# Performance work log

Hardware: AMD Instinct MI355X
Metric: run time of the kernel (lower is better)

## Reference

```python
import jax, jax.numpy as jnp
import numpy as np

N, INC, MID, K = 65536, 256, 64, 16
EPS = 1e-5  # BatchNorm1d default eps


def _bn(x, g, b, m, v):
    # eval-mode BatchNorm1d applied per-channel along the last dim
    return (x - m) * (g * jax.lax.rsqrt(v + EPS)) + b


def setup_inputs() -> dict:
    key = jax.random.key(0)
    ks = jax.random.split(key, 40)
    rn = lambda i, shape, s=0.05: (jax.random.normal(ks[i], shape, jnp.float32) * s)
    pv = lambda i, n: jax.random.uniform(ks[i], (n,), jnp.float32, 0.5, 1.5)  # positive running var
    return {
        "feats": jax.random.normal(ks[0], (N, INC), jnp.float32),
        "pos": jax.random.uniform(ks[1], (N, 3), jnp.float32) * 10.0,
        "idx": jax.random.randint(ks[2], (N, K), 0, N),
        "w_in": rn(3, (MID, INC)),
        "w_q": rn(4, (MID, MID)), "b_q": rn(5, (MID,)),
        "w_k": rn(6, (MID, MID)), "b_k": rn(7, (MID,)),
        "w_v": rn(8, (MID, MID)), "b_v": rn(9, (MID,)),
        # pos_enc: Linear(3,3) -> BN(3) -> ReLU -> Linear(3,mid) -> BN(mid) -> ReLU
        "pe_w1": rn(10, (3, 3)), "pe_b1": rn(11, (3,)),
        "pe_g1": jnp.ones(3), "pe_be1": rn(12, (3,)), "pe_m1": rn(13, (3,)), "pe_v1": pv(14, 3),
        "pe_w2": rn(15, (MID, 3)), "pe_b2": rn(16, (MID,)),
        "pe_g2": jnp.ones(MID), "pe_be2": rn(17, (MID,)), "pe_m2": rn(18, (MID,)), "pe_v2": pv(19, MID),
        # mlp_gamma: Linear(mid,mid) -> BN(mid) -> ReLU -> Linear(mid,mid) -> BN(mid) -> ReLU
        "ga_w1": rn(20, (MID, MID)), "ga_b1": rn(21, (MID,)),
        "ga_g1": jnp.ones(MID), "ga_be1": rn(22, (MID,)), "ga_m1": rn(23, (MID,)), "ga_v1": pv(24, MID),
        "ga_w2": rn(25, (MID, MID)), "ga_b2": rn(26, (MID,)),
        "ga_g2": jnp.ones(MID), "ga_be2": rn(27, (MID,)), "ga_m2": rn(28, (MID,)), "ga_v2": pv(29, MID),
        "w_out": rn(30, (INC, MID)),
    }


def reference(feats, pos, w_in, w_q, b_q, w_k, b_k, w_v, b_v,
              pe_w1, pe_b1, pe_g1, pe_be1, pe_m1, pe_v1,
              pe_w2, pe_b2, pe_g2, pe_be2, pe_m2, pe_v2,
              ga_w1, ga_b1, ga_g1, ga_be1, ga_m1, ga_v1,
              ga_w2, ga_b2, ga_g2, ga_be2, ga_m2, ga_v2,
              w_out, idx):
    xx = feats @ w_in.T                              # [N, mid]
    q = xx @ w_q.T + b_q
    k = xx @ w_k.T + b_k
    v = xx @ w_v.T + b_v
    xv = v[idx]                                      # [N, K, mid] gather
    xk = k[idx]                                      # [N, K, mid]
    xpos = pos[idx]                                  # [N, K, 3]
    # pos_enc
    p = jax.nn.relu(_bn(xpos @ pe_w1.T + pe_b1, pe_g1, pe_be1, pe_m1, pe_v1))
    p = jax.nn.relu(_bn(p @ pe_w2.T + pe_b2, pe_g2, pe_be2, pe_m2, pe_v2))  # [N, K, mid]
    # vector attention logits
    w = xk - q[:, None, :] + p                       # [N, K, mid]
    # mlp_gamma
    w = jax.nn.relu(_bn(w @ ga_w1.T + ga_b1, ga_g1, ga_be1, ga_m1, ga_v1))
    w = jax.nn.relu(_bn(w @ ga_w2.T + ga_b2, ga_g2, ga_be2, ga_m2, ga_v2))
    w = jax.nn.softmax(w, axis=1)                    # softmax over neighbors
    out = jnp.sum((xv + p) * w, axis=1)              # [N, mid]
    out = out @ w_out.T                              # [N, inc]
    return out + feats
```

## Files before the change

kernel.cpp:

```cpp
#include <hip/hip_runtime.h>

#define NPTS 65536
#define INC  256
#define MID  64
#define KNB  16
#define WSTR 72

#define WIN_S   0
#define WQ_S    16384
#define WK_S    20480
#define WV_S    24576
#define GA1_S   28672
#define GA2_S   32768
#define WOUT_S  36864
#define NFRAG_ENT 6656
#define BQ1F_S  53248

typedef __attribute__((ext_vector_type(8))) short short8;
typedef __attribute__((ext_vector_type(4))) float f32x4;

#define MFMA(a, b, c) __builtin_amdgcn_mfma_f32_16x16x32_bf16((a), (b), (c), 0, 0, 0)
#define WBAR() __builtin_amdgcn_wave_barrier()

__device__ inline float bf2f(unsigned short s) {
    unsigned int u = ((unsigned int)s) << 16;
    return __builtin_bit_cast(float, u);
}
__device__ inline unsigned int pk_bf16(float lo, float hi) {
    unsigned int r;
    asm("v_cvt_pk_bf16_f32 %0, %1, %2" : "=v"(r) : "v"(lo), "v"(hi));
    return r;
}
__device__ inline short f2bf(float f) { return (short)pk_bf16(f, f); }

__device__ inline short8 cvtf8(f32x4 a, f32x4 b) {
    union { unsigned int u[4]; short8 s; } r;
    r.u[0] = pk_bf16(a[0], a[1]); r.u[1] = pk_bf16(a[2], a[3]);
    r.u[2] = pk_bf16(b[0], b[1]); r.u[3] = pk_bf16(b[2], b[3]);
    return r.s;
}
__device__ inline short8 load_cvt8(const float* __restrict__ p) {
    const f32x4* v = (const f32x4*)p;
    return cvtf8(v[0], v[1]);
}
__device__ inline short8 load_cvt8s(const float* __restrict__ p, float scale) {
    const f32x4* v = (const f32x4*)p;
    f32x4 a = v[0], b = v[1];
    #pragma unroll
    for (int i = 0; i < 4; i++) { a[i] *= scale; b[i] *= scale; }
    return cvtf8(a, b);
}

__global__ __launch_bounds__(256) void k_prep(
    const float* __restrict__ w_in, const float* __restrict__ w_q,
    const float* __restrict__ w_k, const float* __restrict__ w_v,
    const float* __restrict__ ga_w1, const float* __restrict__ ga_w2,
    const float* __restrict__ w_out, const float* __restrict__ b_q,
    const float* __restrict__ ga_g1, const float* __restrict__ ga_v1,
    const float* __restrict__ ga_b1, const float* __restrict__ ga_be1,
    const float* __restrict__ ga_m1,
    const float* __restrict__ ga_g2, const float* __restrict__ ga_v2,
    short* __restrict__ wbuf)
{
    int gid = blockIdx.x * 256 + threadIdx.x;
    if (gid >= NFRAG_ENT + 64) return;
    if (gid < 2048) {
        int e = gid, f = e >> 6, ln = e & 63;
        int nt = f & 3, ks = f >> 2;
        int row = nt * 16 + (ln & 15), col = ks * 32 + (ln >> 4) * 8;
        *(short8*)&wbuf[(size_t)gid * 8] = load_cvt8(w_in + (size_t)row * INC + col);
    } else if (gid < 4608) {
        int seg = (gid - 2048) >> 9;
        int e = (gid - 2048) & 511;
        int f = e >> 6, ln = e & 63;
        int nt = f & 3, ks = f >> 2;
        int row = nt * 16 + (ln & 15), col = ks * 32 + (ln >> 4) * 8;
        if (seg == 0) {
            float s1r = ga_g1[row] * rsqrtf(ga_v1[row] + 1e-5f);
            float accv[8];
            #pragma unroll
            for (int o = 0; o < 8; o++) accv[o] = 0.f;
            for (int c = 0; c < 64; c++) {
                float a = ga_w1[(size_t)row * MID + c] * s1r;
                #pragma unroll
                for (int o = 0; o < 8; o++)
                    accv[o] += a * w_q[(size_t)c * MID + col + o];
            }
            f32x4 lo = {accv[0], accv[1], accv[2], accv[3]};
            f32x4 hi = {accv[4], accv[5], accv[6], accv[7]};
            *(short8*)&wbuf[(size_t)gid * 8] = cvtf8(lo, hi);
        } else {
            const float* m = seg == 1 ? w_k : seg == 2 ? w_v
                           : seg == 3 ? ga_w1 : ga_w2;
            float scale = 1.f;
            if (seg == 3)      scale = ga_g1[row] * rsqrtf(ga_v1[row] + 1e-5f);
            else if (seg == 4) scale = ga_g2[row] * rsqrtf(ga_v2[row] + 1e-5f);
            *(short8*)&wbuf[(size_t)gid * 8] = load_cvt8s(m + (size_t)row * MID + col, scale);
        }
    } else if (gid < NFRAG_ENT) {
        int e = gid - 4608, f = e >> 6, ln = e & 63;
        int nt = f >> 1, ks = f & 1;
        int row = nt * 16 + (ln & 15), col = ks * 32 + (ln >> 4) * 8;
        *(short8*)&wbuf[(size_t)gid * 8] = load_cvt8(w_out + (size_t)row * MID + col);
    } else {
        int ch = gid - NFRAG_ENT;
        float s1r = ga_g1[ch] * rsqrtf(ga_v1[ch] + 1e-5f);
        float acc = 0.f;
        for (int c = 0; c < 64; c++) acc += ga_w1[(size_t)ch * MID + c] * b_q[c];
        float beta1 = (ga_b1[ch] - ga_m1[ch]) * s1r + ga_be1[ch];
        ((float*)(wbuf + BQ1F_S))[ch] = s1r * acc - beta1;
    }
}

__global__ __launch_bounds__(256) void k_qkv(
    const float* __restrict__ feats, const short* __restrict__ wfrag,
    const float* __restrict__ pos,
    const float* __restrict__ b_k, const float* __restrict__ b_v,
    const float* __restrict__ pe_w1, const float* __restrict__ pe_b1,
    const float* __restrict__ pe_g1, const float* __restrict__ pe_be1,
    const float* __restrict__ pe_m1, const float* __restrict__ pe_v1,
    const float* __restrict__ pe_w2, const float* __restrict__ pe_b2,
    const float* __restrict__ pe_g2, const float* __restrict__ pe_be2,
    const float* __restrict__ pe_m2, const float* __restrict__ pe_v2,
    short* __restrict__ q1f_out, unsigned* __restrict__ kv_out)
{
    __shared__ __align__(16) short XL[4][16 * WSTR];
    __shared__ float PS[4][16 * 4];
    const int tid = threadIdx.x;
    const int wave = tid >> 6, lane = tid & 63;
    const int l15 = lane & 15, quad = lane >> 4;
    const int rb = (blockIdx.x * 4 + wave) * 16;

    if (lane < 16) {
        float s0 = pe_g1[0] * rsqrtf(pe_v1[0] + 1e-5f);
        float s1 = pe_g1[1] * rsqrtf(pe_v1[1] + 1e-5f);
        float sc = pe_g1[2] * rsqrtf(pe_v1[2] + 1e-5f);
        float px = pos[(size_t)(rb + lane) * 3 + 0];
        float py = pos[(size_t)(rb + lane) * 3 + 1];
        float pz = pos[(size_t)(rb + lane) * 3 + 2];
        PS[wave][lane * 4 + 0] =
            fmaxf((px * pe_w1[0] + py * pe_w1[1] + pz * pe_w1[2] + pe_b1[0] - pe_m1[0]) * s0 + pe_be1[0], 0.f);
        PS[wave][lane * 4 + 1] =
            fmaxf((px * pe_w1[3] + py * pe_w1[4] + pz * pe_w1[5] + pe_b1[1] - pe_m1[1]) * s1 + pe_be1[1], 0.f);
        PS[wave][lane * 4 + 2] =
            fmaxf((px * pe_w1[6] + py * pe_w1[7] + pz * pe_w1[8] + pe_b1[2] - pe_m1[2]) * sc + pe_be1[2], 0.f);
    }

    const float* bq1f = (const float*)(wfrag + BQ1F_S);
    float w2c0[4], w2c1[4], w2c2[4], s2c[4], sh2c[4], bq1c[4], bkc[4], bvc[4];
    #pragma unroll
    for (int nt = 0; nt < 4; nt++) {
        int ch = nt * 16 + l15;
        w2c0[nt] = pe_w2[ch * 3 + 0]; w2c1[nt] = pe_w2[ch * 3 + 1]; w2c2[nt] = pe_w2[ch * 3 + 2];
        float s2 = pe_g2[ch] * rsqrtf(pe_v2[ch] + 1e-5f);
        s2c[nt] = s2;
        sh2c[nt] = (pe_b2[ch] - pe_m2[ch]) * s2 + pe_be2[ch];
        bq1c[nt] = bq1f[ch];
        bkc[nt] = b_k[ch]; bvc[nt] = b_v[ch];
    }

    f32x4 acc[4];
    #pragma unroll
    for (int nt = 0; nt < 4; nt++) acc[nt] = (f32x4){0.f, 0.f, 0.f, 0.f};
    const float* arow = feats + (size_t)(rb + l15) * INC + quad * 8;
    #pragma unroll
    for (int ks = 0; ks < 8; ks++) {
        short8 a = load_cvt8(arow + ks * 32);
        #pragma unroll
        for (int nt = 0; nt < 4; nt++) {
            short8 b = *(const short8*)&wfrag[WIN_S + (size_t)((ks * 4 + nt) * 64 + lane) * 8];
            acc[nt] = MFMA(a, b, acc[nt]);
        }
    }
    #pragma unroll
    for (int nt = 0; nt < 4; nt++) {
        unsigned int p01 = pk_bf16(acc[nt][0], acc[nt][1]);
        unsigned int p23 = pk_bf16(acc[nt][2], acc[nt][3]);
        XL[wave][(quad * 4 + 0) * WSTR + nt * 16 + l15] = (short)p01;
        XL[wave][(quad * 4 + 1) * WSTR + nt * 16 + l15] = (short)(p01 >> 16);
        XL[wave][(quad * 4 + 2) * WSTR + nt * 16 + l15] = (short)p23;
        XL[wave][(quad * 4 + 3) * WSTR + nt * 16 + l15] = (short)(p23 >> 16);
    }
    WBAR();
    short8 a0 = *(const short8*)&XL[wave][l15 * WSTR + quad * 8];
    short8 a1 = *(const short8*)&XL[wave][l15 * WSTR + 32 + quad * 8];
    WBAR();

    float p10[4], p11[4], p12[4];
    #pragma unroll
    for (int r = 0; r < 4; r++) {
        p10[r] = PS[wave][(quad * 4 + r) * 4 + 0];
        p11[r] = PS[wave][(quad * 4 + r) * 4 + 1];
        p12[r] = PS[wave][(quad * 4 + r) * 4 + 2];
    }
    float pe_[4][4];
    #pragma unroll
    for (int nt = 0; nt < 4; nt++)
        #pragma unroll
        for (int r = 0; r < 4; r++)
            pe_[nt][r] = fmaxf((p10[r] * w2c0[nt] + p11[r] * w2c1[nt] + p12[r] * w2c2[nt])
                               * s2c[nt] + sh2c[nt], 0.f);

    #pragma unroll
    for (int nt = 0; nt < 4; nt++) {
        short8 b0 = *(const short8*)&wfrag[WQ_S + (size_t)((nt) * 64 + lane) * 8];
        short8 b1 = *(const short8*)&wfrag[WQ_S + (size_t)((4 + nt) * 64 + lane) * 8];
        f32x4 c = (f32x4){0.f, 0.f, 0.f, 0.f};
        c = MFMA(a0, b0, c); c = MFMA(a1, b1, c);
        unsigned int p01 = pk_bf16(c[0] + bq1c[nt], c[1] + bq1c[nt]);
        unsigned int p23 = pk_bf16(c[2] + bq1c[nt], c[3] + bq1c[nt]);
        q1f_out[(unsigned)(rb + quad * 4 + 0) * 64u + nt * 16 + l15] = (short)p01;
        q1f_out[(unsigned)(rb + quad * 4 + 1) * 64u + nt * 16 + l15] = (short)(p01 >> 16);
        q1f_out[(unsigned)(rb + quad * 4 + 2) * 64u + nt * 16 + l15] = (short)p23;
        q1f_out[(unsigned)(rb + quad * 4 + 3) * 64u + nt * 16 + l15] = (short)(p23 >> 16);
    }

    WBAR();
    #pragma unroll
    for (int nt = 0; nt < 4; nt++) {
        short8 b0 = *(const short8*)&wfrag[WK_S + (size_t)((nt) * 64 + lane) * 8];
        short8 b1 = *(const short8*)&wfrag[WK_S + (size_t)((4 + nt) * 64 + lane) * 8];
        f32x4 c = (f32x4){0.f, 0.f, 0.f, 0.f};
        c = MFMA(a0, b0, c); c = MFMA(a1, b1, c);
        unsigned int p01 = pk_bf16(c[0] + bkc[nt] + pe_[nt][0], c[1] + bkc[nt] + pe_[nt][1]);
        unsigned int p23 = pk_bf16(c[2] + bkc[nt] + pe_[nt][2], c[3] + bkc[nt] + pe_[nt][3]);
        XL[wave][(quad * 4 + 0) * WSTR + nt * 16 + l15] = (short)p01;
        XL[wave][(quad * 4 + 1) * WSTR + nt * 16 + l15] = (short)(p01 >> 16);
        XL[wave][(quad * 4 + 2) * WSTR + nt * 16 + l15] = (short)p23;
        XL[wave][(quad * 4 + 3) * WSTR + nt * 16 + l15] = (short)(p23 >> 16);
    }
    WBAR();
    short8 ak0 = *(const short8*)&XL[wave][l15 * WSTR + quad * 8];
    short8 ak1 = *(const short8*)&XL[wave][l15 * WSTR + 32 + quad * 8];
    WBAR();
    float k1f[4][4];
    #pragma unroll
    for (int nt = 0; nt < 4; nt++) {
        short8 b0 = *(const short8*)&wfrag[GA1_S + (size_t)((nt) * 64 + lane) * 8];
        short8 b1 = *(const short8*)&wfrag[GA1_S + (size_t)((4 + nt) * 64 + lane) * 8];
        f32x4 c = (f32x4){0.f, 0.f, 0.f, 0.f};
        c = MFMA(ak0, b0, c); c = MFMA(ak1, b1, c);
        #pragma unroll
        for (int r = 0; r < 4; r++) k1f[nt][r] = c[r];
    }

    #pragma unroll
    for (int nt = 0; nt < 4; nt++) {
        short8 b0 = *(const short8*)&wfrag[WV_S + (size_t)((nt) * 64 + lane) * 8];
        short8 b1 = *(const short8*)&wfrag[WV_S + (size_t)((4 + nt) * 64 + lane) * 8];
        f32x4 c = (f32x4){0.f, 0.f, 0.f, 0.f};
        c = MFMA(a0, b0, c); c = MFMA(a1, b1, c);
        #pragma unroll
        for (int r = 0; r < 4; r++) {
            float vv = c[r] + bvc[nt] + pe_[nt][r];
            kv_out[(unsigned)(rb + quad * 4 + r) * 64u + nt * 16 + l15] =
                pk_bf16(k1f[nt][r], vv);
        }
    }
}

#define GATHER(KVN, IT2)                                                      \
    _Pragma("unroll")                                                         \
    for (int j = 0; j < KNB; j++) {                                           \
        int mj = __builtin_amdgcn_readlane(m_all, (IT2) * 16 + j);            \
        KVN[j] = kvbuf[(unsigned)mj * 64u + (unsigned)lane];                  \
    }

#define ATTN_POINT(IT, KV, QV, WB)                                            \
    {                                                                         \
        short* wb_ = (WB);                                                    \
        _Pragma("unroll")                                                     \
        for (int j = 0; j < KNB; j += 2) {                                    \
            float h0 = fmaxf(__builtin_bit_cast(float, KV[j] << 16) - (QV), 0.f);     \
            float h1 = fmaxf(__builtin_bit_cast(float, KV[j + 1] << 16) - (QV), 0.f); \
            unsigned pkw = pk_bf16(h0, h1);                                   \
            wb_[(j) * WSTR + lane] = (short)pkw;                              \
            wb_[(j + 1) * WSTR + lane] = (short)(pkw >> 16);                  \
        }                                                                     \
        short8 c0 = *(const short8*)&wb_[l15 * WSTR + quad * 8];              \
        short8 c1 = *(const short8*)&wb_[l15 * WSTR + 32 + quad * 8];         \
        float smv[4][4];                                                      \
        _Pragma("unroll")                                                     \
        for (int nt = 0; nt < 4; nt++) {                                      \
            short8 b0 = *(const short8*)&BW[(size_t)((nt) * 64 + lane) * 8];  \
            short8 b1 = *(const short8*)&BW[(size_t)((4 + nt) * 64 + lane) * 8]; \
            f32x4 c = (f32x4){0.f, 0.f, 0.f, 0.f};                            \
            c = MFMA(c0, b0, c); c = MFMA(c1, b1, c);                         \
            float b2v = B2[nt * 16 + l15];                                    \
            _Pragma("unroll")                                                 \
            for (int r = 0; r < 4; r++)                                       \
                smv[nt][r] = fmaxf(c[r] + b2v, 0.f);                          \
        }                                                                     \
        float sarr[4];                                                        \
        _Pragma("unroll")                                                     \
        for (int nt = 0; nt < 4; nt++) {                                      \
            float e0 = __expf(smv[nt][0]), e1 = __expf(smv[nt][1]);           \
            float e2 = __expf(smv[nt][2]), e3 = __expf(smv[nt][3]);           \
            float s = e0 + e1 + e2 + e3;                                      \
            s += __shfl_xor(s, 16);                                           \
            s += __shfl_xor(s, 32);                                           \
            sarr[nt] = s;                                                     \
            unsigned p01 = pk_bf16(e0, e1);                                   \
            unsigned p23 = pk_bf16(e2, e3);                                   \
            wb_[(quad * 4 + 0) * WSTR + nt * 16 + l15] = (short)p01;          \
            wb_[(quad * 4 + 1) * WSTR + nt * 16 + l15] = (short)(p01 >> 16);  \
            wb_[(quad * 4 + 2) * WSTR + nt * 16 + l15] = (short)p23;          \
            wb_[(quad * 4 + 3) * WSTR + nt * 16 + l15] = (short)(p23 >> 16);  \
        }                                                                     \
        float oacc = 0.f;                                                     \
        _Pragma("unroll")                                                     \
        for (int j = 0; j < KNB; j++)                                         \
            oacc += __builtin_bit_cast(float, KV[j] & 0xffff0000u)            \
                    * bf2f((unsigned short)wb_[j * WSTR + lane]);             \
        float s01 = (quad == 0) ? sarr[0] : sarr[1];                          \
        float s23 = (quad == 2) ? sarr[2] : sarr[3];                          \
        float ssel = (quad < 2) ? s01 : s23;                                  \
        OM[((IT) * 4 + wave) * WSTR + lane] = f2bf(oacc * (1.0f / ssel));     \
    }

__global__ __launch_bounds__(256) void k_attn(
    const int* __restrict__ idx,
    const unsigned short* __restrict__ q1f,
    const unsigned* __restrict__ kvbuf, const short* __restrict__ wfrag,
    const float* __restrict__ ga_b2, const float* __restrict__ ga_g2,
    const float* __restrict__ ga_be2, const float* __restrict__ ga_m2,
    const float* __restrict__ ga_v2,
    const float* __restrict__ feats, float* __restrict__ out)
{
    __shared__ __align__(16) short BW[512 * 8];
    __shared__ __align__(16) short Wb[4][2][16 * WSTR];
    __shared__ __align__(16) short OM[16 * WSTR];
    __shared__ float B2[64];

    const int tid = threadIdx.x;
    const int wave = tid >> 6, lane = tid & 63;
    const int l15 = lane & 15, quad = lane >> 4;

    #pragma unroll
    for (int rep = 0; rep < 2; rep++) {
        int e = rep * 256 + tid;
        *(short8*)&BW[(size_t)e * 8] = *(const short8*)&wfrag[GA2_S + (size_t)e * 8];
    }
    if (tid < 64) {
        float s2 = ga_g2[tid] * rsqrtf(ga_v2[tid] + 1e-5f);
        B2[tid] = ga_b2[tid] * s2 + ga_be2[tid] - ga_m2[tid] * s2;
    }
    __syncthreads();

    const int n0 = blockIdx.x * 16 + wave;
    int m_all = idx[(unsigned)(n0 + (lane >> 4) * 4) * 16u + (unsigned)(lane & 15)];
    float qf0 = bf2f(q1f[(unsigned)(n0     ) * 64u + lane]);
    float qf1 = bf2f(q1f[(unsigned)(n0 +  4) * 64u + lane]);
    float qf2 = bf2f(q1f[(unsigned)(n0 +  8) * 64u + lane]);
    float qf3 = bf2f(q1f[(unsigned)(n0 + 12) * 64u + lane]);

    unsigned kvA[KNB], kvB[KNB];
    GATHER(kvA, 0)
    GATHER(kvB, 1)
    ATTN_POINT(0, kvA, qf0, &Wb[wave][0][0])
    GATHER(kvA, 2)
    ATTN_POINT(1, kvB, qf1, &Wb[wave][1][0])
    GATHER(kvB, 3)
    ATTN_POINT(2, kvA, qf2, &Wb[wave][0][0])
    ATTN_POINT(3, kvB, qf3, &Wb[wave][1][0])

    __syncthreads();
    short8 A0 = *(const short8*)&OM[l15 * WSTR + quad * 8];
    short8 A1 = *(const short8*)&OM[l15 * WSTR + 32 + quad * 8];
    const int rb = blockIdx.x * 16;
    #pragma unroll
    for (int t = 0; t < 4; t++) {
        int nt = wave * 4 + t;
        short8 b0 = *(const short8*)&wfrag[WOUT_S + (size_t)((nt * 2 + 0) * 64 + lane) * 8];
        short8 b1 = *(const short8*)&wfrag[WOUT_S + (size_t)((nt * 2 + 1) * 64 + lane) * 8];
        f32x4 c = (f32x4){0.f, 0.f, 0.f, 0.f};
        c = MFMA(A0, b0, c);
        c = MFMA(A1, b1, c);
        #pragma unroll
        for (int r = 0; r < 4; r++) {
            size_t off = (size_t)(rb + quad * 4 + r) * INC + nt * 16 + l15;
            out[off] = c[r] + feats[off];
        }
    }
}

extern "C" void kernel_launch(void* const* d_in, const int* in_sizes, int n_in,
                              void* d_out, int out_size, void* d_ws, size_t ws_size,
                              hipStream_t stream)
{
    const float* feats = (const float*)d_in[0];
    const float* pos   = (const float*)d_in[1];
    const int*   idx   = (const int*)d_in[2];
    const float* w_in  = (const float*)d_in[3];
    const float* w_q   = (const float*)d_in[4];
    const float* b_q   = (const float*)d_in[5];
    const float* w_k   = (const float*)d_in[6];
    const float* b_k   = (const float*)d_in[7];
    const float* w_v   = (const float*)d_in[8];
    const float* b_v   = (const float*)d_in[9];
    const float* pe_w1 = (const float*)d_in[10];
    const float* pe_b1 = (const float*)d_in[11];
    const float* pe_g1 = (const float*)d_in[12];
    const float* pe_be1= (const float*)d_in[13];
    const float* pe_m1 = (const float*)d_in[14];
    const float* pe_v1 = (const float*)d_in[15];
    const float* pe_w2 = (const float*)d_in[16];
    const float* pe_b2 = (const float*)d_in[17];
    const float* pe_g2 = (const float*)d_in[18];
    const float* pe_be2= (const float*)d_in[19];
    const float* pe_m2 = (const float*)d_in[20];
    const float* pe_v2 = (const float*)d_in[21];
    const float* ga_w1 = (const float*)d_in[22];
    const float* ga_b1 = (const float*)d_in[23];
    const float* ga_g1 = (const float*)d_in[24];
    const float* ga_be1= (const float*)d_in[25];
    const float* ga_m1 = (const float*)d_in[26];
    const float* ga_v1 = (const float*)d_in[27];
    const float* ga_w2 = (const float*)d_in[28];
    const float* ga_b2 = (const float*)d_in[29];
    const float* ga_g2 = (const float*)d_in[30];
    const float* ga_be2= (const float*)d_in[31];
    const float* ga_m2 = (const float*)d_in[32];
    const float* ga_v2 = (const float*)d_in[33];
    const float* w_out = (const float*)d_in[34];

    char* ws = (char*)d_ws;
    short*    q1f  = (short*)(ws);
    unsigned* kv   = (unsigned*)(ws + (size_t) 8 * 1024 * 1024);
    short*    wbuf = (short*)(ws + (size_t)24 * 1024 * 1024);

    k_prep<<<27, 256, 0, stream>>>(w_in, w_q, w_k, w_v, ga_w1, ga_w2, w_out, b_q,
                                   ga_g1, ga_v1, ga_b1, ga_be1, ga_m1,
                                   ga_g2, ga_v2, wbuf);
    k_qkv<<<NPTS / 64, 256, 0, stream>>>(feats, wbuf, pos, b_k, b_v,
                                         pe_w1, pe_b1, pe_g1, pe_be1, pe_m1, pe_v1,
                                         pe_w2, pe_b2, pe_g2, pe_be2, pe_m2, pe_v2,
                                         q1f, kv);
    k_attn<<<NPTS / 16, 256, 0, stream>>>(idx,
                                          (const unsigned short*)q1f, kv, wbuf,
                                          ga_b2, ga_g2, ga_be2, ga_m2, ga_v2,
                                          feats, (float*)d_out);
}
```

Measured before the change: 249.4 us.

## Fold log2e into gamma weights, use raw v_exp, drop LDS weight staging

Folds the log2(e) factor into the second mlp_gamma layer weights and bias so the softmax can use the hardware exp2 instruction directly instead of __expf. Removes the shared-memory staging of the second-layer weight fragments and bias, reading the fragments from global memory (relying on cache) and holding the bias in registers. This drops a block-wide barrier and LDS traffic at the cost of repeated global/L2 loads of the weight fragments inside the per-point loop.

Result: slower. 268.8 us (+7.7%).

```diff
diff --git a/kernel.cpp b/kernel.cpp
--- a/kernel.cpp
+++ b/kernel.cpp
@@ -16,6 +16,8 @@
 #define NFRAG_ENT 6656
 #define BQ1F_S  53248
 
+#define LOG2E 1.44269504088896340736f
+
 typedef __attribute__((ext_vector_type(8))) short short8;
 typedef __attribute__((ext_vector_type(4))) float f32x4;
 
@@ -32,6 +34,11 @@
     return r;
 }
 __device__ inline short f2bf(float f) { return (short)pk_bf16(f, f); }
+__device__ inline float exp2fast(float x) {
+    float r;
+    asm("v_exp_f32 %0, %1" : "=v"(r) : "v"(x));
+    return r;
+}
 
 __device__ inline short8 cvtf8(f32x4 a, f32x4 b) {
     union { unsigned int u[4]; short8 s; } r;
@@ -94,7 +101,7 @@
                            : seg == 3 ? ga_w1 : ga_w2;
             float scale = 1.f;
             if (seg == 3)      scale = ga_g1[row] * rsqrtf(ga_v1[row] + 1e-5f);
-            else if (seg == 4) scale = ga_g2[row] * rsqrtf(ga_v2[row] + 1e-5f);
+            else if (seg == 4) scale = ga_g2[row] * rsqrtf(ga_v2[row] + 1e-5f) * LOG2E;
             *(short8*)&wbuf[(size_t)gid * 8] = load_cvt8s(m + (size_t)row * MID + col, scale);
         }
     } else if (gid < NFRAG_ENT) {
@@ -282,20 +289,19 @@
         float smv[4][4];                                                      \
         _Pragma("unroll")                                                     \
         for (int nt = 0; nt < 4; nt++) {                                      \
-            short8 b0 = *(const short8*)&BW[(size_t)((nt) * 64 + lane) * 8];  \
-            short8 b1 = *(const short8*)&BW[(size_t)((4 + nt) * 64 + lane) * 8]; \
+            short8 b0 = *(const short8*)&wfrag[GA2_S + (size_t)((nt) * 64 + lane) * 8];     \
+            short8 b1 = *(const short8*)&wfrag[GA2_S + (size_t)((4 + nt) * 64 + lane) * 8]; \
             f32x4 c = (f32x4){0.f, 0.f, 0.f, 0.f};                            \
             c = MFMA(c0, b0, c); c = MFMA(c1, b1, c);                         \
-            float b2v = B2[nt * 16 + l15];                                    \
             _Pragma("unroll")                                                 \
             for (int r = 0; r < 4; r++)                                       \
-                smv[nt][r] = fmaxf(c[r] + b2v, 0.f);                          \
+                smv[nt][r] = fmaxf(c[r] + b2c[nt], 0.f);                      \
         }                                                                     \
         float sarr[4];                                                        \
         _Pragma("unroll")                                                     \
         for (int nt = 0; nt < 4; nt++) {                                      \
-            float e0 = __expf(smv[nt][0]), e1 = __expf(smv[nt][1]);           \
-            float e2 = __expf(smv[nt][2]), e3 = __expf(smv[nt][3]);           \
+            float e0 = exp2fast(smv[nt][0]), e1 = exp2fast(smv[nt][1]);       \
+            float e2 = exp2fast(smv[nt][2]), e3 = exp2fast(smv[nt][3]);       \
             float s = e0 + e1 + e2 + e3;                                      \
             s += __shfl_xor(s, 16);                                           \
             s += __shfl_xor(s, 32);                                           \
@@ -327,25 +333,19 @@
     const float* __restrict__ ga_v2,
     const float* __restrict__ feats, float* __restrict__ out)
 {
-    __shared__ __align__(16) short BW[512 * 8];
     __shared__ __align__(16) short Wb[4][2][16 * WSTR];
     __shared__ __align__(16) short OM[16 * WSTR];
-    __shared__ float B2[64];
-
     const int tid = threadIdx.x;
     const int wave = tid >> 6, lane = tid & 63;
     const int l15 = lane & 15, quad = lane >> 4;
 
-    #pragma unroll
-    for (int rep = 0; rep < 2; rep++) {
-        int e = rep * 256 + tid;
-        *(short8*)&BW[(size_t)e * 8] = *(const short8*)&wfrag[GA2_S + (size_t)e * 8];
-    }
-    if (tid < 64) {
-        float s2 = ga_g2[tid] * rsqrtf(ga_v2[tid] + 1e-5f);
-        B2[tid] = ga_b2[tid] * s2 + ga_be2[tid] - ga_m2[tid] * s2;
-    }
-    __syncthreads();
+    float b2c[4];
+    #pragma unroll
+    for (int nt = 0; nt < 4; nt++) {
+        int ch = nt * 16 + l15;
+        float s2 = ga_g2[ch] * rsqrtf(ga_v2[ch] + 1e-5f);
+        b2c[nt] = (ga_b2[ch] * s2 + ga_be2[ch] - ga_m2[ch] * s2) * LOG2E;
+    }
 
     const int n0 = blockIdx.x * 16 + wave;
     int m_all = idx[(unsigned)(n0 + (lane >> 4) * 4) * 16u + (unsigned)(lane & 15)];
```
